# Kernel tuning notes

Measured on AMD Instinct MI355X. Metric: run time of the kernel, lower is better.

## Reference

```python
import jax, jax.numpy as jnp
import numpy as np

HEAD_SIZE = 64


def setup_inputs() -> dict:
    key = jax.random.key(0)
    kx, kq, kk, kv = jax.random.split(key, 4)
    B, L, D = 4, 4096, 1024
    scale = 1.0 / np.sqrt(D)
    x = jax.random.normal(kx, (B, L, D), dtype=jnp.float32)
    Wq = jax.random.normal(kq, (D, HEAD_SIZE), dtype=jnp.float32) * scale
    Wk = jax.random.normal(kk, (D, HEAD_SIZE), dtype=jnp.float32) * scale
    Wv = jax.random.normal(kv, (D, HEAD_SIZE), dtype=jnp.float32) * scale
    return {"x": x, "Wq": Wq, "Wk": Wk, "Wv": Wv}


def reference(x, Wq, Wk, Wv):
    B, L, D = x.shape
    H = Wq.shape[1]
    q = jnp.einsum('bld,dh->blh', x, Wq)  # [B,L,H]
    k = jnp.einsum('bld,dh->blh', x, Wk)
    v = jnp.einsum('bld,dh->blh', x, Wv)
    # full L x L score matrix, as in the original module
    scores = jnp.einsum('bqh,bkh->bqk', q, k) / jnp.sqrt(jnp.float32(H))
    causal = jnp.tril(jnp.ones((L, L), dtype=bool))
    scores = jnp.where(causal, scores, -jnp.inf)
    attn = jax.nn.softmax(scores, axis=-1)
    z = jnp.einsum('bqk,bkh->bqh', attn, v)  # [B,L,H]
    return z
```

## Files before the change

### kernel.cpp

```cpp
#include <hip/hip_runtime.h>
#include <stdint.h>

#define L_SEQ 4096
#define D_MODEL 1024
#define HEAD 64
#define KCH 512
#define MAXCH 8
#define NQT 32

typedef unsigned short u16;
typedef _Float16 f16;
typedef __attribute__((ext_vector_type(8))) f16 f16x8;
typedef __attribute__((ext_vector_type(2))) __fp16 fp16x2;
typedef __attribute__((ext_vector_type(4))) float f32x4;

static __device__ __forceinline__ u16 f16bits(float f) {
    union { f16 h; u16 u; } c; c.h = (f16)f; return c.u;
}
static __device__ __forceinline__ uint32_t pk16(float a, float b) {
    union { fp16x2 h; uint32_t u; } c;
    c.h = __builtin_amdgcn_cvt_pkrtz(a, b);
    return c.u;
}
static __device__ __forceinline__ f16x8 ld8h(const u16* p) { return *(const f16x8*)p; }

static __device__ __forceinline__ f32x4 mfma16h(f16x8 a, f16x8 b, f32x4 c) {
    return __builtin_amdgcn_mfma_f32_16x16x32_f16(a, b, c, 0, 0, 0);
}

static __device__ __forceinline__ void gload16(const u16* g, u16* l) {
    __builtin_amdgcn_global_load_lds(
        (const __attribute__((address_space(1))) void*)g,
        (__attribute__((address_space(3))) void*)l, 16, 0, 0);
}

static __device__ __forceinline__ int Sq(int qt) {
    int f = qt >> 2, r = qt & 3;
    return (f + 1) * (2 * f + r);
}

__global__ __launch_bounds__(256) void conv_w(
    const float* __restrict__ Wq, const float* __restrict__ Wk,
    const float* __restrict__ Wv, u16* __restrict__ Wt)
{
    __shared__ u16 tile[64][72];
    const float* W = (blockIdx.y == 0) ? Wq : (blockIdx.y == 1) ? Wk : Wv;
    const float sc = (blockIdx.y == 0) ? 0.18033688f : 1.0f;
    u16* dst = Wt + blockIdx.y * (HEAD * D_MODEL);
    const int k0 = blockIdx.x * 64, t = threadIdx.x;
    #pragma unroll
    for (int i = 0; i < 16; i++) {
        int idx = i * 256 + t;
        int kk = idx >> 6, h = idx & 63;
        tile[h][kk] = f16bits(W[(size_t)(k0 + kk) * HEAD + h] * sc);
    }
    __syncthreads();
    #pragma unroll
    for (int i = 0; i < 16; i++) {
        int idx = i * 256 + t;
        int h = idx >> 6, kk = idx & 63;
        dst[(size_t)h * D_MODEL + k0 + kk] = tile[h][kk];
    }
}

__global__ __launch_bounds__(256, 4) void qkv_proj(
    const float* __restrict__ x, const u16* __restrict__ Wt,
    u16* __restrict__ qb, u16* __restrict__ kb, u16* __restrict__ vTb)
{
    __shared__ __align__(16) u16 Wl[2 * 192 * 32];
    __shared__ __align__(16) u16 Xl[2 * 32 * 36];
#define WLX(dh,r,c) Wl[((dh)*192 + (r))*32 + (c)]
#define XLX(kh,r,c) Xl[((kh)*32  + (r))*36 + (c)]
#define CT(r,c)     Wl[(r)*200 + (c)]

    const int t = threadIdx.x;
    const int wv = t >> 6, lane = t & 63;
    const int ln16 = lane & 15, quad = lane >> 4;
    const int w3 = wv * 3;
    const int m0 = blockIdx.x * 32;

    f32x4 acc[2][3] = {};
    float4 xv0, xv1;

    auto issueW = [&](int s) {
        const int k0 = s * 64;
        #pragma unroll
        for (int k2 = 0; k2 < 6; k2++) {
            int c = wv * 6 + k2;
            int dh = c & 1, g = c >> 1;
            const u16* gp = Wt + (size_t)(g * 16 + (lane >> 2)) * D_MODEL
                               + k0 + dh * 32 + (lane & 3) * 8;
            gload16(gp, &WLX(dh, g * 16 + (lane >> 2), (lane & 3) * 8));
        }
    };
    auto loadx = [&](int s) {
        const int k0 = s * 64;
        int r0 = t >> 4, cs0 = (t & 15) * 4;
        xv0 = *(const float4*)&x[(size_t)(m0 + r0) * D_MODEL + k0 + cs0];
        int idx = 256 + t, r1 = idx >> 4, cs1 = (idx & 15) * 4;
        xv1 = *(const float4*)&x[(size_t)(m0 + r1) * D_MODEL + k0 + cs1];
    };
    auto packx = [&]() {
        int r0 = t >> 4, cs0 = (t & 15) * 4;
        uint2 p0; p0.x = pk16(xv0.x, xv0.y); p0.y = pk16(xv0.z, xv0.w);
        *(uint2*)&XLX(cs0 >> 5, r0, cs0 & 31) = p0;
        int idx = 256 + t, r1 = idx >> 4, cs1 = (idx & 15) * 4;
        uint2 p1; p1.x = pk16(xv1.x, xv1.y); p1.y = pk16(xv1.z, xv1.w);
        *(uint2*)&XLX(cs1 >> 5, r1, cs1 & 31) = p1;
    };

    loadx(0); issueW(0); packx();
    for (int s = 0; s < 16; s++) {
        __syncthreads();
        f16x8 xb[2][2], af[2][3];
        #pragma unroll
        for (int c = 0; c < 2; c++) {
            xb[c][0] = ld8h(&XLX(c, ln16, quad * 8));
            xb[c][1] = ld8h(&XLX(c, 16 + ln16, quad * 8));
            #pragma unroll
            for (int j = 0; j < 3; j++)
                af[c][j] = ld8h(&WLX(c, (w3 + j) * 16 + ln16, quad * 8));
        }
        #pragma unroll
        for (int c = 0; c < 2; c++)
            #pragma unroll
            for (int j = 0; j < 3; j++) {
                acc[0][j] = mfma16h(af[c][j], xb[c][0], acc[0][j]);
                acc[1][j] = mfma16h(af[c][j], xb[c][1], acc[1][j]);
            }
        if (s + 1 < 16) loadx(s + 1);
        __syncthreads();
        if (s + 1 < 16) { issueW(s + 1); packx(); }
    }

    __syncthreads();
    #pragma unroll
    for (int mt = 0; mt < 2; mt++) {
        #pragma unroll
        for (int j = 0; j < 3; j++) {
            int g0 = (w3 + j) * 16 + quad * 4;
            uint2 pk;
            pk.x = pk16(acc[mt][j][0], acc[mt][j][1]);
            pk.y = pk16(acc[mt][j][2], acc[mt][j][3]);
            *(uint2*)&CT(mt * 16 + ln16, g0) = pk;
        }
    }
    __syncthreads();
    {
        int m = t >> 3, hg = (t & 7) * 8;
        *(f16x8*)&qb[(size_t)(m0 + m) * HEAD + hg] = *(f16x8*)&CT(m, hg);
        *(f16x8*)&kb[(size_t)(m0 + m) * HEAD + hg] = *(f16x8*)&CT(m, 64 + hg);
        int h = t >> 2, mg = (t & 3) * 8;
        f16x8 vvv;
        #pragma unroll
        for (int jj = 0; jj < 8; jj++)
            ((u16*)&vvv)[jj] = CT(mg + jj, 128 + h);
        int bbt = m0 >> 12, l0 = m0 & 4095;
        *(f16x8*)&vTb[(size_t)(bbt * HEAD + h) * L_SEQ + l0 + mg] = vvv;
    }
#undef WLX
#undef XLX
#undef CT
}

__global__ __launch_bounds__(256, 4) void attn_chunk(
    const u16* __restrict__ qb, const u16* __restrict__ kb,
    const u16* __restrict__ vT, float* __restrict__ Opart, float* __restrict__ lpart)
{
    const int qt = blockIdx.x, ch = blockIdx.y, b = blockIdx.z;
    if (ch * KCH > qt * 128 + 127) return;

    __shared__ __align__(16) u16 Kls[2 * 64 * 32];
    __shared__ __align__(16) u16 Vls[2 * 64 * 32];
    __shared__ __align__(16) u16 Pls[4 * 32 * 72];
#define KBX(dh,r,c) Kls[((dh)*64 + (r))*32 + (c)]
#define VBX(kh,r,c) Vls[((kh)*64 + (r))*32 + (c)]
#define PX(r,c)     Pls[((wv)*32 + (r))*72 + (c)]

    const int t = threadIdx.x, wv = t >> 6, lane = t & 63;
    const int ln16 = lane & 15, quad = lane >> 4;
    const int qmin = qt * 128 + wv * 32;

    f16x8 qf[2][2];
    #pragma unroll
    for (int qn = 0; qn < 2; qn++) {
        const u16* qrp = qb + (size_t)(b * L_SEQ + qmin + qn * 16 + ln16) * HEAD + quad * 8;
        qf[qn][0] = ld8h(qrp); qf[qn][1] = ld8h(qrp + 32);
    }

    const u16* kbb = kb + (size_t)b * L_SEQ * HEAD;
    const u16* vbb = vT + (size_t)b * HEAD * L_SEQ;

    f32x4 o[2][4] = {};
    float lsum[2] = {0.f, 0.f};

    const int kv_lo = ch * KCH;
    const int kv_hi = min(kv_lo + KCH, qt * 128 + 128);
    const int nst = (kv_hi - kv_lo) >> 6;

    auto issue_stage = [&](int kv0) {
        #pragma unroll
        for (int k2 = 0; k2 < 4; k2++) {
            int c = wv * 4 + k2;
            if (c < 8) {
                int dh = c & 1, g = c >> 1;
                const u16* gp = kbb + (size_t)(kv0 + g * 16 + (lane >> 2)) * HEAD
                                    + dh * 32 + (lane & 3) * 8;
                gload16(gp, &KBX(dh, g * 16 + (lane >> 2), (lane & 3) * 8));
            } else {
                int c2 = c - 8, kh = c2 & 1, g = c2 >> 1;
                const u16* gp = vbb + (size_t)(g * 16 + (lane >> 2)) * L_SEQ
                                    + kv0 + kh * 32 + (lane & 3) * 8;
                gload16(gp, &VBX(kh, g * 16 + (lane >> 2), (lane & 3) * 8));
            }
        }
    };

    for (int s = 0; s < nst; s++) {
        const int kv0 = kv_lo + s * 64;
        issue_stage(kv0);
        __syncthreads();

        #pragma unroll
        for (int g = 0; g < 4; g++) {
            f16x8 ka0 = ld8h(&KBX(0, g * 16 + ln16, quad * 8));
            f16x8 ka1 = ld8h(&KBX(1, g * 16 + ln16, quad * 8));
            #pragma unroll
            for (int qn = 0; qn < 2; qn++) {
                f32x4 s2 = {};
                s2 = mfma16h(ka0, qf[qn][0], s2);
                s2 = mfma16h(ka1, qf[qn][1], s2);
                float p0, p1, p2, p3;
                if (kv0 + g * 16 + 15 <= qmin + qn * 16) {
                    p0 = __builtin_amdgcn_exp2f(s2[0]);
                    p1 = __builtin_amdgcn_exp2f(s2[1]);
                    p2 = __builtin_amdgcn_exp2f(s2[2]);
                    p3 = __builtin_amdgcn_exp2f(s2[3]);
                } else {
                    int q = qmin + qn * 16 + ln16;
                    int kv = kv0 + g * 16 + quad * 4;
                    p0 = (kv     <= q) ? __builtin_amdgcn_exp2f(s2[0]) : 0.f;
                    p1 = (kv + 1 <= q) ? __builtin_amdgcn_exp2f(s2[1]) : 0.f;
                    p2 = (kv + 2 <= q) ? __builtin_amdgcn_exp2f(s2[2]) : 0.f;
                    p3 = (kv + 3 <= q) ? __builtin_amdgcn_exp2f(s2[3]) : 0.f;
                }
                lsum[qn] += (p0 + p1) + (p2 + p3);
                uint2 pk; pk.x = pk16(p0, p1); pk.y = pk16(p2, p3);
                *(uint2*)&PX(qn * 16 + ln16, g * 16 + quad * 4) = pk;
            }
        }
        f16x8 pf[2][2];
        #pragma unroll
        for (int qn = 0; qn < 2; qn++) {
            pf[qn][0] = ld8h(&PX(qn * 16 + ln16, quad * 8));
            pf[qn][1] = ld8h(&PX(qn * 16 + ln16, 32 + quad * 8));
        }
        #pragma unroll
        for (int hg = 0; hg < 4; hg++) {
            f16x8 va0 = ld8h(&VBX(0, hg * 16 + ln16, quad * 8));
            f16x8 va1 = ld8h(&VBX(1, hg * 16 + ln16, quad * 8));
            #pragma unroll
            for (int qn = 0; qn < 2; qn++) {
                o[qn][hg] = mfma16h(va0, pf[qn][0], o[qn][hg]);
                o[qn][hg] = mfma16h(va1, pf[qn][1], o[qn][hg]);
            }
        }
        __syncthreads();
    }

    #pragma unroll
    for (int qn = 0; qn < 2; qn++) {
        lsum[qn] += __shfl_xor(lsum[qn], 16);
        lsum[qn] += __shfl_xor(lsum[qn], 32);
    }

    const size_t base = (size_t)(b * 144 + Sq(qt) + ch);
    #pragma unroll
    for (int qn = 0; qn < 2; qn++) {
        int q_local = wv * 32 + qn * 16 + ln16;
        #pragma unroll
        for (int hg = 0; hg < 4; hg++)
            *(f32x4*)&Opart[base * 8192 + (size_t)q_local * 64 + hg * 16 + quad * 4] = o[qn][hg];
        if (quad == 0)
            lpart[base * 128 + q_local] = lsum[qn];
    }
#undef KBX
#undef VBX
#undef PX
}

__global__ __launch_bounds__(256) void merge_chunks(
    const float* __restrict__ Opart, const float* __restrict__ lpart,
    float* __restrict__ out)
{
    const int qt = blockIdx.x, qseg = blockIdx.y, b = blockIdx.z;
    const int nch = (qt + 4) >> 2;
    const int t = threadIdx.x;
    const size_t obase = (size_t)(b * 144 + Sq(qt)) * 8192;
    const size_t lbase = (size_t)(b * 144 + Sq(qt)) * 128;
    #pragma unroll
    for (int i = 0; i < 2; i++) {
        int idx = i * 256 + t;
        int q = qseg * 32 + (idx >> 4), hg = (idx & 15) * 4;
        float L = 0.f, ax = 0.f, ay = 0.f, az = 0.f, aw = 0.f;
        #pragma unroll
        for (int c = 0; c < MAXCH; c++) {
            if (c < nch) {
                L += lpart[lbase + c * 128 + q];
                const float4 v = *(const float4*)&Opart[obase + (size_t)c * 8192 + q * 64 + hg];
                ax += v.x; ay += v.y; az += v.z; aw += v.w;
            }
        }
        float inv = 1.f / L;
        float4 r; r.x = ax * inv; r.y = ay * inv; r.z = az * inv; r.w = aw * inv;
        *(float4*)&out[((size_t)(b * L_SEQ + qt * 128 + q)) * HEAD + hg] = r;
    }
}

extern "C" void kernel_launch(void* const* d_in, const int* in_sizes, int n_in,
                              void* d_out, int out_size, void* d_ws, size_t ws_size,
                              hipStream_t stream) {
    const float* x  = (const float*)d_in[0];
    const float* Wq = (const float*)d_in[1];
    const float* Wk = (const float*)d_in[2];
    const float* Wv = (const float*)d_in[3];
    float* out = (float*)d_out;

    u16* ws16 = (u16*)d_ws;
    u16* Wt  = ws16;
    u16* qb  = Wt + 3 * HEAD * D_MODEL;
    u16* kb  = qb + 16384 * HEAD;
    u16* vTb = kb + 16384 * HEAD;
    float* Opart = (float*)(vTb + 16384 * HEAD);
    float* lpart = Opart + (size_t)4 * 144 * 8192;

    conv_w      <<<dim3(16, 3), 256, 0, stream>>>(Wq, Wk, Wv, Wt);
    qkv_proj    <<<dim3(512), 256, 0, stream>>>(x, Wt, qb, kb, vTb);
    attn_chunk  <<<dim3(NQT, MAXCH, 4), 256, 0, stream>>>(qb, kb, vTb, Opart, lpart);
    merge_chunks<<<dim3(NQT, 4, 4), 256, 0, stream>>>(Opart, lpart, out);
}
```

Before: 151.8 us.

## Double-buffer LDS tiles in projection and attention kernels to prefetch next stage

Both the QKV projection and the attention chunk kernel now keep two LDS buffers for the W and K/V tiles. Each iteration issues the global-to-LDS load for the next stage before computing on the current one, so load latency can overlap with MFMA work. The extra LDS lowers the launch-bounds occupancy hint from 4 to 3 blocks per CU, trading latency hiding from concurrent blocks for in-block prefetch. The barrier at the end of each iteration still waits on the outstanding loads, which limits how much overlap is possible.

```diff
diff --git a/kernel.cpp b/kernel.cpp
--- a/kernel.cpp
+++ b/kernel.cpp
@@ -63,15 +63,15 @@
     }
 }
 
-__global__ __launch_bounds__(256, 4) void qkv_proj(
+__global__ __launch_bounds__(256, 3) void qkv_proj(
     const float* __restrict__ x, const u16* __restrict__ Wt,
     u16* __restrict__ qb, u16* __restrict__ kb, u16* __restrict__ vTb)
 {
-    __shared__ __align__(16) u16 Wl[2 * 192 * 32];
+    __shared__ __align__(16) u16 Wl[2][2 * 192 * 32];
     __shared__ __align__(16) u16 Xl[2 * 32 * 36];
-#define WLX(dh,r,c) Wl[((dh)*192 + (r))*32 + (c)]
+#define WLX(bf,dh,r,c) Wl[bf][((dh)*192 + (r))*32 + (c)]
 #define XLX(kh,r,c) Xl[((kh)*32  + (r))*36 + (c)]
-#define CT(r,c)     Wl[(r)*200 + (c)]
+#define CT(r,c)     Wl[0][(r)*200 + (c)]
 
     const int t = threadIdx.x;
     const int wv = t >> 6, lane = t & 63;
@@ -82,7 +82,7 @@
     f32x4 acc[2][3] = {};
     float4 xv0, xv1;
 
-    auto issueW = [&](int s) {
+    auto issueW = [&](int s, int bf) {
         const int k0 = s * 64;
         #pragma unroll
         for (int k2 = 0; k2 < 6; k2++) {
@@ -90,7 +90,7 @@
             int dh = c & 1, g = c >> 1;
             const u16* gp = Wt + (size_t)(g * 16 + (lane >> 2)) * D_MODEL
                                + k0 + dh * 32 + (lane & 3) * 8;
-            gload16(gp, &WLX(dh, g * 16 + (lane >> 2), (lane & 3) * 8));
+            gload16(gp, &WLX(bf, dh, g * 16 + (lane >> 2), (lane & 3) * 8));
         }
     };
     auto loadx = [&](int s) {
@@ -109,9 +109,11 @@
         *(uint2*)&XLX(cs1 >> 5, r1, cs1 & 31) = p1;
     };
 
-    loadx(0); issueW(0); packx();
+    loadx(0); issueW(0, 0); packx();
     for (int s = 0; s < 16; s++) {
+        const int bf = s & 1;
         __syncthreads();
+        if (s + 1 < 16) issueW(s + 1, bf ^ 1);
         f16x8 xb[2][2], af[2][3];
         #pragma unroll
         for (int c = 0; c < 2; c++) {
@@ -119,7 +121,7 @@
             xb[c][1] = ld8h(&XLX(c, 16 + ln16, quad * 8));
             #pragma unroll
             for (int j = 0; j < 3; j++)
-                af[c][j] = ld8h(&WLX(c, (w3 + j) * 16 + ln16, quad * 8));
+                af[c][j] = ld8h(&WLX(bf, c, (w3 + j) * 16 + ln16, quad * 8));
         }
         #pragma unroll
         for (int c = 0; c < 2; c++)
@@ -130,7 +132,7 @@
             }
         if (s + 1 < 16) loadx(s + 1);
         __syncthreads();
-        if (s + 1 < 16) { issueW(s + 1); packx(); }
+        if (s + 1 < 16) packx();
     }
 
     __syncthreads();
@@ -163,18 +165,18 @@
 #undef CT
 }
 
-__global__ __launch_bounds__(256, 4) void attn_chunk(
+__global__ __launch_bounds__(256, 3) void attn_chunk(
     const u16* __restrict__ qb, const u16* __restrict__ kb,
     const u16* __restrict__ vT, float* __restrict__ Opart, float* __restrict__ lpart)
 {
     const int qt = blockIdx.x, ch = blockIdx.y, b = blockIdx.z;
     if (ch * KCH > qt * 128 + 127) return;
 
-    __shared__ __align__(16) u16 Kls[2 * 64 * 32];
-    __shared__ __align__(16) u16 Vls[2 * 64 * 32];
+    __shared__ __align__(16) u16 Kls[2][2 * 64 * 32];
+    __shared__ __align__(16) u16 Vls[2][2 * 64 * 32];
     __shared__ __align__(16) u16 Pls[4 * 32 * 72];
-#define KBX(dh,r,c) Kls[((dh)*64 + (r))*32 + (c)]
-#define VBX(kh,r,c) Vls[((kh)*64 + (r))*32 + (c)]
+#define KBX(bf,dh,r,c) Kls[bf][((dh)*64 + (r))*32 + (c)]
+#define VBX(bf,kh,r,c) Vls[bf][((kh)*64 + (r))*32 + (c)]
 #define PX(r,c)     Pls[((wv)*32 + (r))*72 + (c)]
 
     const int t = threadIdx.x, wv = t >> 6, lane = t & 63;
@@ -198,7 +200,7 @@
     const int kv_hi = min(kv_lo + KCH, qt * 128 + 128);
     const int nst = (kv_hi - kv_lo) >> 6;
 
-    auto issue_stage = [&](int kv0) {
+    auto issue_stage = [&](int kv0, int bf) {
         #pragma unroll
         for (int k2 = 0; k2 < 4; k2++) {
             int c = wv * 4 + k2;
@@ -206,25 +208,27 @@
                 int dh = c & 1, g = c >> 1;
                 const u16* gp = kbb + (size_t)(kv0 + g * 16 + (lane >> 2)) * HEAD
                                     + dh * 32 + (lane & 3) * 8;
-                gload16(gp, &KBX(dh, g * 16 + (lane >> 2), (lane & 3) * 8));
+                gload16(gp, &KBX(bf, dh, g * 16 + (lane >> 2), (lane & 3) * 8));
             } else {
                 int c2 = c - 8, kh = c2 & 1, g = c2 >> 1;
                 const u16* gp = vbb + (size_t)(g * 16 + (lane >> 2)) * L_SEQ
                                     + kv0 + kh * 32 + (lane & 3) * 8;
-                gload16(gp, &VBX(kh, g * 16 + (lane >> 2), (lane & 3) * 8));
+                gload16(gp, &VBX(bf, kh, g * 16 + (lane >> 2), (lane & 3) * 8));
             }
         }
     };
 
+    issue_stage(kv_lo, 0);
+    __syncthreads();
     for (int s = 0; s < nst; s++) {
+        const int bf = s & 1;
         const int kv0 = kv_lo + s * 64;
-        issue_stage(kv0);
-        __syncthreads();
+        if (s + 1 < nst) issue_stage(kv0 + 64, bf ^ 1);
 
         #pragma unroll
         for (int g = 0; g < 4; g++) {
-            f16x8 ka0 = ld8h(&KBX(0, g * 16 + ln16, quad * 8));
-            f16x8 ka1 = ld8h(&KBX(1, g * 16 + ln16, quad * 8));
+            f16x8 ka0 = ld8h(&KBX(bf, 0, g * 16 + ln16, quad * 8));
+            f16x8 ka1 = ld8h(&KBX(bf, 1, g * 16 + ln16, quad * 8));
             #pragma unroll
             for (int qn = 0; qn < 2; qn++) {
                 f32x4 s2 = {};
@@ -257,8 +261,8 @@
         }
         #pragma unroll
         for (int hg = 0; hg < 4; hg++) {
-            f16x8 va0 = ld8h(&VBX(0, hg * 16 + ln16, quad * 8));
-            f16x8 va1 = ld8h(&VBX(1, hg * 16 + ln16, quad * 8));
+            f16x8 va0 = ld8h(&VBX(bf, 0, hg * 16 + ln16, quad * 8));
+            f16x8 va1 = ld8h(&VBX(bf, 1, hg * 16 + ln16, quad * 8));
             #pragma unroll
             for (int qn = 0; qn < 2; qn++) {
                 o[qn][hg] = mfma16h(va0, pf[qn][0], o[qn][hg]);
```

New measurement: 160.0 us. 5.4% more time.

## Fuse chunk merge into attention kernel via last-block atomic counter

Applied to the files above, without the earlier changes.

Removes the separate merge_chunks launch. Each attention block writes its partial O and l, then bumps a per-(batch, query-tile) atomic counter, and the last-arriving block sums all chunks and writes the final output. Query tiles with a single chunk skip the partial buffers and write normalized output directly. Counters are zeroed in conv_w. This saves a kernel launch and some partial-buffer traffic, at the cost of fences, atomics and a serialized merge tail in the last block.

```diff
diff --git a/kernel.cpp b/kernel.cpp
--- a/kernel.cpp
+++ b/kernel.cpp
@@ -41,13 +41,14 @@
 
 __global__ __launch_bounds__(256) void conv_w(
     const float* __restrict__ Wq, const float* __restrict__ Wk,
-    const float* __restrict__ Wv, u16* __restrict__ Wt)
+    const float* __restrict__ Wv, u16* __restrict__ Wt, int* __restrict__ cnt)
 {
     __shared__ u16 tile[64][72];
     const float* W = (blockIdx.y == 0) ? Wq : (blockIdx.y == 1) ? Wk : Wv;
     const float sc = (blockIdx.y == 0) ? 0.18033688f : 1.0f;
     u16* dst = Wt + blockIdx.y * (HEAD * D_MODEL);
     const int k0 = blockIdx.x * 64, t = threadIdx.x;
+    if (blockIdx.x == 0 && blockIdx.y == 0 && t < 128) cnt[t] = 0;
     #pragma unroll
     for (int i = 0; i < 16; i++) {
         int idx = i * 256 + t;
@@ -165,7 +166,8 @@
 
 __global__ __launch_bounds__(256, 4) void attn_chunk(
     const u16* __restrict__ qb, const u16* __restrict__ kb,
-    const u16* __restrict__ vT, float* __restrict__ Opart, float* __restrict__ lpart)
+    const u16* __restrict__ vT, float* __restrict__ Opart, float* __restrict__ lpart,
+    float* __restrict__ out, int* __restrict__ cnt)
 {
     const int qt = blockIdx.x, ch = blockIdx.y, b = blockIdx.z;
     if (ch * KCH > qt * 128 + 127) return;
@@ -173,6 +175,7 @@
     __shared__ __align__(16) u16 Kls[2 * 64 * 32];
     __shared__ __align__(16) u16 Vls[2 * 64 * 32];
     __shared__ __align__(16) u16 Pls[4 * 32 * 72];
+    __shared__ int lastf;
 #define KBX(dh,r,c) Kls[((dh)*64 + (r))*32 + (c)]
 #define VBX(kh,r,c) Vls[((kh)*64 + (r))*32 + (c)]
 #define PX(r,c)     Pls[((wv)*32 + (r))*72 + (c)]
@@ -180,6 +183,7 @@
     const int t = threadIdx.x, wv = t >> 6, lane = t & 63;
     const int ln16 = lane & 15, quad = lane >> 4;
     const int qmin = qt * 128 + wv * 32;
+    const int nch = (qt + 4) >> 2;
 
     f16x8 qf[2][2];
     #pragma unroll
@@ -274,6 +278,22 @@
         lsum[qn] += __shfl_xor(lsum[qn], 32);
     }
 
+    if (nch == 1) {
+        #pragma unroll
+        for (int qn = 0; qn < 2; qn++) {
+            float inv = 1.f / lsum[qn];
+            int q = qmin + qn * 16 + ln16;
+            #pragma unroll
+            for (int hg = 0; hg < 4; hg++) {
+                float4 r;
+                r.x = o[qn][hg][0] * inv; r.y = o[qn][hg][1] * inv;
+                r.z = o[qn][hg][2] * inv; r.w = o[qn][hg][3] * inv;
+                *(float4*)&out[((size_t)(b * L_SEQ + q)) * HEAD + hg * 16 + quad * 4] = r;
+            }
+        }
+        return;
+    }
+
     const size_t base = (size_t)(b * 144 + Sq(qt) + ch);
     #pragma unroll
     for (int qn = 0; qn < 2; qn++) {
@@ -284,24 +304,23 @@
         if (quad == 0)
             lpart[base * 128 + q_local] = lsum[qn];
     }
-#undef KBX
-#undef VBX
-#undef PX
-}
-
-__global__ __launch_bounds__(256) void merge_chunks(
-    const float* __restrict__ Opart, const float* __restrict__ lpart,
-    float* __restrict__ out)
-{
-    const int qt = blockIdx.x, qseg = blockIdx.y, b = blockIdx.z;
-    const int nch = (qt + 4) >> 2;
-    const int t = threadIdx.x;
+
+    __syncthreads();
+    if (t == 0) {
+        __threadfence();
+        int old = atomicAdd(&cnt[b * 32 + qt], 1);
+        lastf = (old == nch - 1);
+    }
+    __syncthreads();
+    if (!lastf) return;
+    __threadfence();
+
     const size_t obase = (size_t)(b * 144 + Sq(qt)) * 8192;
     const size_t lbase = (size_t)(b * 144 + Sq(qt)) * 128;
     #pragma unroll
-    for (int i = 0; i < 2; i++) {
+    for (int i = 0; i < 8; i++) {
         int idx = i * 256 + t;
-        int q = qseg * 32 + (idx >> 4), hg = (idx & 15) * 4;
+        int q = idx >> 4, hg = (idx & 15) * 4;
         float L = 0.f, ax = 0.f, ay = 0.f, az = 0.f, aw = 0.f;
         #pragma unroll
         for (int c = 0; c < MAXCH; c++) {
@@ -315,6 +334,9 @@
         float4 r; r.x = ax * inv; r.y = ay * inv; r.z = az * inv; r.w = aw * inv;
         *(float4*)&out[((size_t)(b * L_SEQ + qt * 128 + q)) * HEAD + hg] = r;
     }
+#undef KBX
+#undef VBX
+#undef PX
 }
 
 extern "C" void kernel_launch(void* const* d_in, const int* in_sizes, int n_in,
@@ -333,9 +355,9 @@
     u16* vTb = kb + 16384 * HEAD;
     float* Opart = (float*)(vTb + 16384 * HEAD);
     float* lpart = Opart + (size_t)4 * 144 * 8192;
-
-    conv_w      <<<dim3(16, 3), 256, 0, stream>>>(Wq, Wk, Wv, Wt);
+    int*   cnt   = (int*)(lpart + (size_t)4 * 144 * 128);
+
+    conv_w      <<<dim3(16, 3), 256, 0, stream>>>(Wq, Wk, Wv, Wt, cnt);
     qkv_proj    <<<dim3(512), 256, 0, stream>>>(x, Wt, qb, kb, vTb);
-    attn_chunk  <<<dim3(NQT, MAXCH, 4), 256, 0, stream>>>(qb, kb, vTb, Opart, lpart);
-    merge_chunks<<<dim3(NQT, 4, 4), 256, 0, stream>>>(Opart, lpart, out);
-}
+    attn_chunk  <<<dim3(NQT, MAXCH, 4), 256, 0, stream>>>(qb, kb, vTb, Opart, lpart, out, cnt);
+}
```

After: 201.5 us. 1.33x slower.

## Overlap next K/V tile loads with compute and write single-chunk tiles directly

Applied to the files above, without the earlier changes.

Splits the per-stage K/V load into separate K and V issues. The next K tile is prefetched after the score phase and the next V tile after the PV phase, so global-to-LDS loads overlap with compute instead of being issued right before a barrier. Query tiles that need only one KV chunk now normalize and write the output directly from the attention kernel, and the merge kernel skips those tiles. This removes some partial-buffer traffic and merge work. Each stage keeps two barriers, and correctness depends on the ordering of K/V buffer reuse with the barriers.

```diff
diff --git a/kernel.cpp b/kernel.cpp
--- a/kernel.cpp
+++ b/kernel.cpp
@@ -165,7 +165,8 @@
 
 __global__ __launch_bounds__(256, 4) void attn_chunk(
     const u16* __restrict__ qb, const u16* __restrict__ kb,
-    const u16* __restrict__ vT, float* __restrict__ Opart, float* __restrict__ lpart)
+    const u16* __restrict__ vT, float* __restrict__ Opart, float* __restrict__ lpart,
+    float* __restrict__ out)
 {
     const int qt = blockIdx.x, ch = blockIdx.y, b = blockIdx.z;
     if (ch * KCH > qt * 128 + 127) return;
@@ -180,6 +181,7 @@
     const int t = threadIdx.x, wv = t >> 6, lane = t & 63;
     const int ln16 = lane & 15, quad = lane >> 4;
     const int qmin = qt * 128 + wv * 32;
+    const int nch = (qt + 4) >> 2;
 
     f16x8 qf[2][2];
     #pragma unroll
@@ -198,28 +200,32 @@
     const int kv_hi = min(kv_lo + KCH, qt * 128 + 128);
     const int nst = (kv_hi - kv_lo) >> 6;
 
-    auto issue_stage = [&](int kv0) {
-        #pragma unroll
-        for (int k2 = 0; k2 < 4; k2++) {
-            int c = wv * 4 + k2;
-            if (c < 8) {
-                int dh = c & 1, g = c >> 1;
-                const u16* gp = kbb + (size_t)(kv0 + g * 16 + (lane >> 2)) * HEAD
-                                    + dh * 32 + (lane & 3) * 8;
-                gload16(gp, &KBX(dh, g * 16 + (lane >> 2), (lane & 3) * 8));
-            } else {
-                int c2 = c - 8, kh = c2 & 1, g = c2 >> 1;
-                const u16* gp = vbb + (size_t)(g * 16 + (lane >> 2)) * L_SEQ
-                                    + kv0 + kh * 32 + (lane & 3) * 8;
-                gload16(gp, &VBX(kh, g * 16 + (lane >> 2), (lane & 3) * 8));
-            }
-        }
-    };
+    auto issueK = [&](int kv0) {
+        #pragma unroll
+        for (int k2 = 0; k2 < 2; k2++) {
+            int c = wv * 2 + k2;
+            int dh = c & 1, g = c >> 1;
+            const u16* gp = kbb + (size_t)(kv0 + g * 16 + (lane >> 2)) * HEAD
+                                + dh * 32 + (lane & 3) * 8;
+            gload16(gp, &KBX(dh, g * 16 + (lane >> 2), (lane & 3) * 8));
+        }
+    };
+    auto issueV = [&](int kv0) {
+        #pragma unroll
+        for (int k2 = 0; k2 < 2; k2++) {
+            int c = wv * 2 + k2;
+            int kh = c & 1, g = c >> 1;
+            const u16* gp = vbb + (size_t)(g * 16 + (lane >> 2)) * L_SEQ
+                                + kv0 + kh * 32 + (lane & 3) * 8;
+            gload16(gp, &VBX(kh, g * 16 + (lane >> 2), (lane & 3) * 8));
+        }
+    };
+
+    issueK(kv_lo); issueV(kv_lo);
+    __syncthreads();
 
     for (int s = 0; s < nst; s++) {
         const int kv0 = kv_lo + s * 64;
-        issue_stage(kv0);
-        __syncthreads();
 
         #pragma unroll
         for (int g = 0; g < 4; g++) {
@@ -249,6 +255,10 @@
                 *(uint2*)&PX(qn * 16 + ln16, g * 16 + quad * 4) = pk;
             }
         }
+
+        __syncthreads();
+        if (s + 1 < nst) issueK(kv0 + 64);
+
         f16x8 pf[2][2];
         #pragma unroll
         for (int qn = 0; qn < 2; qn++) {
@@ -265,13 +275,31 @@
                 o[qn][hg] = mfma16h(va1, pf[qn][1], o[qn][hg]);
             }
         }
+
         __syncthreads();
+        if (s + 1 < nst) issueV(kv0 + 64);
     }
 
     #pragma unroll
     for (int qn = 0; qn < 2; qn++) {
         lsum[qn] += __shfl_xor(lsum[qn], 16);
         lsum[qn] += __shfl_xor(lsum[qn], 32);
+    }
+
+    if (nch == 1) {
+        #pragma unroll
+        for (int qn = 0; qn < 2; qn++) {
+            float inv = 1.f / lsum[qn];
+            int q = qmin + qn * 16 + ln16;
+            #pragma unroll
+            for (int hg = 0; hg < 4; hg++) {
+                float4 r;
+                r.x = o[qn][hg][0] * inv; r.y = o[qn][hg][1] * inv;
+                r.z = o[qn][hg][2] * inv; r.w = o[qn][hg][3] * inv;
+                *(float4*)&out[((size_t)(b * L_SEQ + q)) * HEAD + hg * 16 + quad * 4] = r;
+            }
+        }
+        return;
     }
 
     const size_t base = (size_t)(b * 144 + Sq(qt) + ch);
@@ -293,7 +321,7 @@
     const float* __restrict__ Opart, const float* __restrict__ lpart,
     float* __restrict__ out)
 {
-    const int qt = blockIdx.x, qseg = blockIdx.y, b = blockIdx.z;
+    const int qt = blockIdx.x + 4, qseg = blockIdx.y, b = blockIdx.z;
     const int nch = (qt + 4) >> 2;
     const int t = threadIdx.x;
     const size_t obase = (size_t)(b * 144 + Sq(qt)) * 8192;
@@ -336,6 +364,6 @@
 
     conv_w      <<<dim3(16, 3), 256, 0, stream>>>(Wq, Wk, Wv, Wt);
     qkv_proj    <<<dim3(512), 256, 0, stream>>>(x, Wt, qb, kb, vTb);
-    attn_chunk  <<<dim3(NQT, MAXCH, 4), 256, 0, stream>>>(qb, kb, vTb, Opart, lpart);
-    merge_chunks<<<dim3(NQT, 4, 4), 256, 0, stream>>>(Opart, lpart, out);
-}
+    attn_chunk  <<<dim3(NQT, MAXCH, 4), 256, 0, stream>>>(qb, kb, vTb, Opart, lpart, out);
+    merge_chunks<<<dim3(NQT - 4, 4, 4), 256, 0, stream>>>(Opart, lpart, out);
+}
```

Measured after the change: 151.3 us. About the same (-0.3%).
